# Kernel tuning notes

Measured on AMD Instinct MI355X. Metric: run time of the kernel, lower is better.

Reference implementation:

```python
import jax, jax.numpy as jnp
import numpy as np

T, B, N = 1000, 64, 512
DT = 0.01
EL, VR, TR, TINF = -0.07, -0.07, -0.06, -0.05
A_VAL = 2.6239240169525146
A1_VAL = -0.015625353902578354
A2_VAL = -1.0590057373046875
B_VAL = 12.77495288848877
G_VAL = 45.24007797241211
K1, K2 = 200.0, 20.0
R1, R2 = 0.3858567178249359, -1.1421641111373901
C = 1.0


def setup_inputs() -> dict:
    key = jax.random.key(0)
    x = jax.random.normal(key, (T, B, N), dtype=jnp.float32)
    linear = jnp.ones((1, N), jnp.float32)
    a = jnp.full((1, N), A_VAL, jnp.float32)
    A1 = jnp.full((1, N), A1_VAL * C, jnp.float32)
    A2 = jnp.full((1, N), A2_VAL * C, jnp.float32)
    return {"x": x, "linear": linear, "a": a, "A1": A1, "A2": A2}


def _spike(v):
    # Heaviside step (forward of SurrGradSpike)
    return (v > 0).astype(v.dtype)


def reference(x, linear, a, A1, A2):
    G = G_VAL * C

    def step(state, xt):
        V, i1, i2, Thr = state
        i1 = i1 - K1 * i1 * DT
        i2 = i2 - K2 * i2 * DT
        V = V + DT * (linear * xt + i1 + i2 - G * (V - EL)) / C
        Thr = Thr + DT * (a * (V - EL) - B_VAL * (Thr - TINF))
        spk = _spike(V - Thr)
        i1 = (1.0 - spk) * i1 + spk * (R1 * i1 + A1)
        i2 = (1.0 - spk) * i2 + spk * (R2 * i2 + A2)
        Thr = (1.0 - spk) * Thr + spk * jnp.maximum(Thr, TR)
        V = (1.0 - spk) * V + spk * VR
        return (V, i1, i2, Thr), spk

    Bd, Nd = x.shape[1], x.shape[2]
    init = (
        jnp.full((Bd, Nd), EL, x.dtype),   # V
        jnp.zeros((Bd, Nd), x.dtype),      # i1
        jnp.zeros((Bd, Nd), x.dtype),      # i2
        jnp.full((Bd, Nd), TINF, x.dtype), # Thr
    )
    _, spikes = jax.lax.scan(step, init, x)
    return spikes  # [T, B, N] (original returns np.array of per-step spikes)
```

## Files before the change

### kernel.cpp

```cpp
#include <hip/hip_runtime.h>


#define T_STEPS 1000
#define B_DIM 64
#define N_DIM 512
#define BN (B_DIM * N_DIM)

#define C_DT   0.01f
#define C_EL   (-0.07f)
#define C_VR   (-0.07f)
#define C_TR   (-0.06f)
#define C_TINF (-0.05f)
#define C_B    12.77495288848877f
#define C_G    45.24007797241211f
#define C_K1   200.0f
#define C_K2   20.0f
#define C_R1   0.3858567178249359f
#define C_R2   (-1.1421641111373901f)

__device__ __forceinline__ float mn_step(float xt, float lin, float av,
                                         float A1v, float A2v,
                                         float& V, float& i1, float& i2,
                                         float& Thr)
{
#pragma clang fp contract(off)
    i1 = i1 - (C_K1 * i1) * C_DT;
    i2 = i2 - (C_K2 * i2) * C_DT;
    float p  = lin * xt;
    float q  = p + i1;
    float r  = q + i2;
    float e  = V - C_EL;
    float g  = C_G * e;
    float s  = r - g;
    float d  = C_DT * s;
    V = V + d;
    float e2 = V - C_EL;
    float u  = av * e2;
    float w  = Thr - C_TINF;
    float bw = C_B * w;
    float s2 = u - bw;
    float d2 = C_DT * s2;
    Thr = Thr + d2;
    float diff = V - Thr;
    bool  sb   = diff > 0.0f;
    float spk  = sb ? 1.0f : 0.0f;
    float i1r = (C_R1 * i1) + A1v;
    float i2r = (C_R2 * i2) + A2v;
    i1  = sb ? i1r : i1;
    i2  = sb ? i2r : i2;
    float tm = fmaxf(Thr, C_TR);
    Thr = sb ? tm : Thr;
    V   = sb ? C_VR : V;
    return spk;
}

__global__ __launch_bounds__(64) void mn_neuron_kernel(
    const float* __restrict__ x, const float* __restrict__ linear,
    const float* __restrict__ a, const float* __restrict__ A1,
    const float* __restrict__ A2, float* __restrict__ out)
{
#pragma clang fp contract(off)
    const int idx = blockIdx.x * 64 + threadIdx.x;
    const int n   = idx & (N_DIM - 1);

    const float lin = linear[n];
    const float av  = a[n];
    const float A1v = A1[n];
    const float A2v = A2[n];

    float V   = C_EL;
    float i1  = 0.0f;
    float i2  = 0.0f;
    float Thr = C_TINF;

    constexpr int K  = 10;
    constexpr int NC = T_STEPS / K;
    float bufA[K], bufB[K];

    const float* xp = x + idx;
    float*       op = out + idx;

#pragma unroll
    for (int j = 0; j < K; ++j) bufA[j] = xp[(size_t)j * BN];

    for (int c = 0; c < NC; c += 2) {
        {
            const float* p = xp + (size_t)(c + 1) * K * BN;
#pragma unroll
            for (int j = 0; j < K; ++j) bufB[j] = p[(size_t)j * BN];
        }
        {
            float* o = op + (size_t)c * K * BN;
#pragma unroll
            for (int j = 0; j < K; ++j) {
                float spk = mn_step(bufA[j], lin, av, A1v, A2v, V, i1, i2, Thr);
                o[(size_t)j * BN] = spk;
            }
        }
        if (c + 2 < NC) {
            const float* p = xp + (size_t)(c + 2) * K * BN;
#pragma unroll
            for (int j = 0; j < K; ++j) bufA[j] = p[(size_t)j * BN];
        }
        {
            float* o = op + (size_t)(c + 1) * K * BN;
#pragma unroll
            for (int j = 0; j < K; ++j) {
                float spk = mn_step(bufB[j], lin, av, A1v, A2v, V, i1, i2, Thr);
                o[(size_t)j * BN] = spk;
            }
        }
    }
}

extern "C" void kernel_launch(void* const* d_in, const int* in_sizes, int n_in,
                              void* d_out, int out_size, void* d_ws, size_t ws_size,
                              hipStream_t stream) {
    const float* x      = (const float*)d_in[0];
    const float* linear = (const float*)d_in[1];
    const float* a      = (const float*)d_in[2];
    const float* A1     = (const float*)d_in[3];
    const float* A2     = (const float*)d_in[4];
    float* out = (float*)d_out;

    mn_neuron_kernel<<<BN / 64, 64, 0, stream>>>(x, linear, a, A1, A2, out);
}
```

Before: 258.0 us.

## Add producer wavefront streaming x into double-buffered LDS via global_load_lds

```diff
diff --git a/kernel.cpp b/kernel.cpp
--- a/kernel.cpp
+++ b/kernel.cpp
@@ -5,6 +5,9 @@
 #define B_DIM 64
 #define N_DIM 512
 #define BN (B_DIM * N_DIM)
+
+#define K_CHUNK 20
+#define NCHUNK (T_STEPS / K_CHUNK)
 
 #define C_DT   0.01f
 #define C_EL   (-0.07f)
@@ -17,6 +20,9 @@
 #define C_K2   20.0f
 #define C_R1   0.3858567178249359f
 #define C_R2   (-1.1421641111373901f)
+
+typedef const __attribute__((address_space(1))) void* gp_t;
+typedef __attribute__((address_space(3))) void* lp_t;
 
 __device__ __forceinline__ float mn_step(float xt, float lin, float av,
                                          float A1v, float A2v,
@@ -54,61 +60,75 @@
     return spk;
 }
 
-__global__ __launch_bounds__(64) void mn_neuron_kernel(
+__global__ __launch_bounds__(128) void mn_neuron_kernel(
     const float* __restrict__ x, const float* __restrict__ linear,
     const float* __restrict__ a, const float* __restrict__ A1,
     const float* __restrict__ A2, float* __restrict__ out)
 {
 #pragma clang fp contract(off)
-    const int idx = blockIdx.x * 64 + threadIdx.x;
-    const int n   = idx & (N_DIM - 1);
+    __shared__ float lds[2][K_CHUNK][64];
 
-    const float lin = linear[n];
-    const float av  = a[n];
-    const float A1v = A1[n];
-    const float A2v = A2[n];
+    const int lane = threadIdx.x & 63;
+    const int wid  = threadIdx.x >> 6;
+    const int blk  = blockIdx.x;
 
-    float V   = C_EL;
-    float i1  = 0.0f;
-    float i2  = 0.0f;
-    float Thr = C_TINF;
+    if (wid == 1) {
+        const float* pl = x + (size_t)(lane >> 4) * BN
+                            + (size_t)blk * 64 + (size_t)(lane & 15) * 4;
 
-    constexpr int K  = 10;
-    constexpr int NC = T_STEPS / K;
-    float bufA[K], bufB[K];
+        {
+#pragma unroll
+            for (int s = 0; s < K_CHUNK / 4; ++s) {
+                __builtin_amdgcn_global_load_lds(
+                    (gp_t)(pl + (size_t)(s * 4) * BN),
+                    (lp_t)&lds[0][s * 4][0], 16, 0, 0);
+            }
+            __builtin_amdgcn_s_waitcnt(0x0F70);
+        }
+        __syncthreads();
 
-    const float* xp = x + idx;
-    float*       op = out + idx;
+        for (int c = 0; c < NCHUNK; ++c) {
+            if (c + 1 < NCHUNK) {
+                const float* pc = pl + (size_t)((c + 1) * K_CHUNK) * BN;
+                float* dst = &lds[(c + 1) & 1][0][0];
+#pragma unroll
+                for (int s = 0; s < K_CHUNK / 4; ++s) {
+                    __builtin_amdgcn_global_load_lds(
+                        (gp_t)(pc + (size_t)(s * 4) * BN),
+                        (lp_t)(dst + s * 4 * 64), 16, 0, 0);
+                }
+                __builtin_amdgcn_s_waitcnt(0x0F70);
+            }
+            __syncthreads();
+        }
+    } else {
+        const int idx = blk * 64 + lane;
+        const int n   = idx & (N_DIM - 1);
 
+        const float lin = linear[n];
+        const float av  = a[n];
+        const float A1v = A1[n];
+        const float A2v = A2[n];
+
+        float V   = C_EL;
+        float i1  = 0.0f;
+        float i2  = 0.0f;
+        float Thr = C_TINF;
+
+        float* op = out + idx;
+
+        __syncthreads();
+
+        for (int c = 0; c < NCHUNK; ++c) {
+            const float* src = &lds[c & 1][0][lane];
 #pragma unroll
-    for (int j = 0; j < K; ++j) bufA[j] = xp[(size_t)j * BN];
-
-    for (int c = 0; c < NC; c += 2) {
-        {
-            const float* p = xp + (size_t)(c + 1) * K * BN;
-#pragma unroll
-            for (int j = 0; j < K; ++j) bufB[j] = p[(size_t)j * BN];
-        }
-        {
-            float* o = op + (size_t)c * K * BN;
-#pragma unroll
-            for (int j = 0; j < K; ++j) {
-                float spk = mn_step(bufA[j], lin, av, A1v, A2v, V, i1, i2, Thr);
-                o[(size_t)j * BN] = spk;
+            for (int j = 0; j < K_CHUNK; ++j) {
+                float xt  = src[j * 64];
+                float spk = mn_step(xt, lin, av, A1v, A2v, V, i1, i2, Thr);
+                *op = spk;
+                op += BN;
             }
-        }
-        if (c + 2 < NC) {
-            const float* p = xp + (size_t)(c + 2) * K * BN;
-#pragma unroll
-            for (int j = 0; j < K; ++j) bufA[j] = p[(size_t)j * BN];
-        }
-        {
-            float* o = op + (size_t)(c + 1) * K * BN;
-#pragma unroll
-            for (int j = 0; j < K; ++j) {
-                float spk = mn_step(bufB[j], lin, av, A1v, A2v, V, i1, i2, Thr);
-                o[(size_t)j * BN] = spk;
-            }
+            __syncthreads();
         }
     }
 }
@@ -123,5 +143,5 @@
     const float* A2     = (const float*)d_in[4];
     float* out = (float*)d_out;
 
-    mn_neuron_kernel<<<BN / 64, 64, 0, stream>>>(x, linear, a, A1, A2, out);
+    mn_neuron_kernel<<<BN / 64, 128, 0, stream>>>(x, linear, a, A1, A2, out);
 }
```

Result: faster. 234.8 us (-9.0%).
